# Kernel optimization log

Hardware: AMD Instinct MI355X
Metric: run time of the kernel (lower is better)

## Reference

```python
import jax, jax.numpy as jnp
import numpy as np

V, E, G = 25000, 50000, 1024
D_IN, E_IN, D, EH = 74, 12, 64, 128
STEPS, S2S, L, NT = 6, 6, 3, 1


def setup_inputs() -> dict:
    key = jax.random.key(0)
    ks = jax.random.split(key, 20)
    p = lambda k, shp: (jax.random.normal(k, shp, jnp.float32) * 0.05)
    return {
        "node_feats": jax.random.normal(ks[0], (V, D_IN), jnp.float32),
        "edge_feats": jax.random.normal(ks[1], (E, E_IN), jnp.float32),
        "src": jax.random.randint(ks[2], (E,), 0, V),
        "dst": jax.random.randint(ks[3], (E,), 0, V),
        "node2graph": jnp.sort(jax.random.randint(ks[4], (V,), 0, G)),
        "W_proj": p(ks[5], (D_IN, D)), "b_proj": jnp.zeros((D,), jnp.float32),
        "W_e1": p(ks[6], (E_IN, EH)), "b_e1": jnp.zeros((EH,), jnp.float32),
        "W_e2": p(ks[7], (EH, D * D)), "b_e2": jnp.zeros((D * D,), jnp.float32),
        "b_conv": jnp.zeros((D,), jnp.float32),
        "gru_W_ih": p(ks[8], (3 * D, D)), "gru_W_hh": p(ks[9], (3 * D, D)),
        "gru_b_ih": jnp.zeros((3 * D,), jnp.float32), "gru_b_hh": jnp.zeros((3 * D,), jnp.float32),
        "lstm_W_ih0": p(ks[10], (4 * D, 2 * D)), "lstm_W_hh0": p(ks[11], (4 * D, D)),
        "lstm_b_ih0": jnp.zeros((4 * D,), jnp.float32), "lstm_b_hh0": jnp.zeros((4 * D,), jnp.float32),
        "lstm_W_ih_r": p(ks[12], (L - 1, 4 * D, D)), "lstm_W_hh_r": p(ks[13], (L - 1, 4 * D, D)),
        "lstm_b_ih_r": jnp.zeros((L - 1, 4 * D), jnp.float32), "lstm_b_hh_r": jnp.zeros((L - 1, 4 * D), jnp.float32),
        "W1": p(ks[14], (2 * D, D)), "b1": jnp.zeros((D,), jnp.float32),
        "bn_gamma": jnp.ones((D,), jnp.float32), "bn_beta": jnp.zeros((D,), jnp.float32),
        "bn_mean": jnp.zeros((D,), jnp.float32), "bn_var": jnp.ones((D,), jnp.float32),
        "W2": p(ks[15], (D, 4 * NT)), "b2": jnp.zeros((4 * NT,), jnp.float32),
    }


def reference(node_feats, edge_feats, src, dst, node2graph,
              W_proj, b_proj, W_e1, b_e1, W_e2, b_e2, b_conv,
              gru_W_ih, gru_W_hh, gru_b_ih, gru_b_hh,
              lstm_W_ih0, lstm_W_hh0, lstm_b_ih0, lstm_b_hh0,
              lstm_W_ih_r, lstm_W_hh_r, lstm_b_ih_r, lstm_b_hh_r,
              W1, b1, bn_gamma, bn_beta, bn_mean, bn_var, W2, b2):
    # --- MPNNGNN: project + ReLU, then NNConv(sum) + ReLU + GRU, x STEPS ---
    h = jax.nn.relu(node_feats @ W_proj + b_proj)                       # (V, D)
    # edge network: per-edge (D,D) mixing matrix (edge_feats constant across steps)
    We = (jax.nn.relu(edge_feats @ W_e1 + b_e1) @ W_e2 + b_e2).reshape(E, D, D)

    def mp_step(hh, _):
        m = jnp.einsum('ed,edo->eo', hh[src], We)                       # per-edge message
        agg = jax.ops.segment_sum(m, dst, num_segments=V) + b_conv      # NNConv sum + bias
        x = jax.nn.relu(agg)
        gi = x @ gru_W_ih.T + gru_b_ih                                  # GRU (torch gate order r,z,n)
        gh = hh @ gru_W_hh.T + gru_b_hh
        ir, iz, inn = jnp.split(gi, 3, axis=-1)
        hr, hz, hn = jnp.split(gh, 3, axis=-1)
        r = jax.nn.sigmoid(ir + hr)
        z = jax.nn.sigmoid(iz + hz)
        n = jnp.tanh(inn + r * hn)
        return (1.0 - z) * n + z * hh, None

    h, _ = jax.lax.scan(mp_step, h, None, length=STEPS)

    # --- Set2Set readout ---
    q_star = jnp.zeros((G, 2 * D), h.dtype)
    hs = jnp.zeros((L, G, D), h.dtype)
    cs = jnp.zeros((L, G, D), h.dtype)
    for _ in range(S2S):
        x = q_star
        nh, nc = [], []
        for l in range(L):                                              # stacked LSTM, seq len 1
            Wih = lstm_W_ih0 if l == 0 else lstm_W_ih_r[l - 1]
            Whh = lstm_W_hh0 if l == 0 else lstm_W_hh_r[l - 1]
            bih = lstm_b_ih0 if l == 0 else lstm_b_ih_r[l - 1]
            bhh = lstm_b_hh0 if l == 0 else lstm_b_hh_r[l - 1]
            gates = x @ Wih.T + bih + hs[l] @ Whh.T + bhh               # torch order i,f,g,o
            i, f, g, o = jnp.split(gates, 4, axis=-1)
            c = jax.nn.sigmoid(f) * cs[l] + jax.nn.sigmoid(i) * jnp.tanh(g)
            hc = jax.nn.sigmoid(o) * jnp.tanh(c)
            nh.append(hc); nc.append(c)
            x = hc
        hs, cs = jnp.stack(nh), jnp.stack(nc)
        q = x                                                           # (G, D)
        e = jnp.sum(h * q[node2graph], axis=-1)                         # (V,) attention logits
        emax = jax.lax.stop_gradient(jax.ops.segment_max(e, node2graph, num_segments=G))
        emax = jnp.where(jnp.isfinite(emax), emax, 0.0)
        ez = jnp.exp(e - emax[node2graph])                              # per-graph softmax
        denom = jax.ops.segment_sum(ez, node2graph, num_segments=G)
        alpha = ez / jnp.maximum(denom[node2graph], 1e-12)
        readout = jax.ops.segment_sum(h * alpha[:, None], node2graph, num_segments=G)
        q_star = jnp.concatenate([q, readout], axis=-1)                 # (G, 2D)

    # --- evidential head: Linear + ReLU + BatchNorm(eval) + Linear ---
    h1 = jax.nn.relu(q_star @ W1 + b1)
    hbn = bn_gamma * (h1 - bn_mean) * jax.lax.rsqrt(bn_var + 1e-5) + bn_beta
    out = hbn @ W2 + b2                                                 # (G, 4*NT)
    means, logl, loga, logb = jnp.split(out, 4, axis=1)
    MINV = 1e-6
    lam = jax.nn.softplus(logl) + MINV
    alp = jax.nn.softplus(loga) + MINV + 1.0
    bet = jax.nn.softplus(logb) + MINV
    return jnp.stack([means, lam, alp, bet], axis=2).reshape(out.shape)
```

## Files before the change

kernel.cpp:

```cpp
#include <hip/hip_runtime.h>
#include <stdint.h>

#define V_N 25000
#define E_N 50000
#define G_N 1024
#define DIN 74
#define EIN 12
#define NSTEPS 6
#define NS2S 6
#define MPAD 50176

typedef unsigned int u32;
typedef unsigned short u16;
typedef __attribute__((ext_vector_type(8))) short bf16x8v;
typedef __attribute__((ext_vector_type(4))) float f32x4v;

typedef __attribute__((address_space(3))) void lds_void;
typedef __attribute__((address_space(1))) void gbl_void;

__device__ __forceinline__ void gload_lds16(const void* g, void* l) {
  __builtin_amdgcn_global_load_lds((gbl_void*)g, (lds_void*)l, 16, 0, 0);
}

__device__ __forceinline__ u16 f2bf(float f) {
  u32 u = __float_as_uint(f);
  u = (u + 0x7fffu + ((u >> 16) & 1u)) >> 16;
  return (u16)u;
}
__device__ __forceinline__ u32 pack2bf(float lo, float hi) {
  return (u32)f2bf(lo) | ((u32)f2bf(hi) << 16);
}
__device__ __forceinline__ float bflo(u32 w){ return __uint_as_float(w << 16); }
__device__ __forceinline__ float bfhi(u32 w){ return __uint_as_float(w & 0xffff0000u); }
__device__ __forceinline__ float bf2f(u16 v){ return __uint_as_float(((u32)v) << 16); }
__device__ __forceinline__ float sigf(float x){ return 1.f/(1.f + expf(-x)); }
__device__ __forceinline__ float splusf(float x){ return fmaxf(x, 0.f) + log1pf(expf(-fabsf(x))); }

__global__ void prep_kernel(const float* gWih, const float* gWhh,
                            const float* lWih0, const float* lWhh0,
                            const float* lWihr, const float* lWhhr,
                            const float* We2,
                            float* gWihT, float* gWhhT,
                            u32* TW40, u32* TU40, u32* TW4r, u32* TU4r,
                            u16* WbT) {
  int idx = blockIdx.x * 256 + threadIdx.x;
  if (idx < 12288) { int d = idx / 192, r = idx % 192; gWihT[idx] = gWih[r*64 + d]; return; }
  idx -= 12288;
  if (idx < 12288) { int d = idx / 192, r = idx % 192; gWhhT[idx] = gWhh[r*64 + d]; return; }
  idx -= 12288;
  if (idx < 16384) { int q = idx >> 2, j = idx & 3; int k8 = q >> 8, r = q & 255;
                     TW40[idx] = pack2bf(lWih0[r*128 + k8*8 + 2*j], lWih0[r*128 + k8*8 + 2*j + 1]); return; }
  idx -= 16384;
  if (idx < 8192)  { int q = idx >> 2, j = idx & 3; int k8 = q >> 8, r = q & 255;
                     TU40[idx] = pack2bf(lWhh0[r*64 + k8*8 + 2*j], lWhh0[r*64 + k8*8 + 2*j + 1]); return; }
  idx -= 8192;
  if (idx < 16384) { int l = idx >> 13, rem = idx & 8191; int q = rem >> 2, j = rem & 3;
                     int k8 = q >> 8, r = q & 255;
                     TW4r[idx] = pack2bf(lWihr[l*16384 + r*64 + k8*8 + 2*j],
                                         lWihr[l*16384 + r*64 + k8*8 + 2*j + 1]); return; }
  idx -= 16384;
  if (idx < 16384) { int l = idx >> 13, rem = idx & 8191; int q = rem >> 2, j = rem & 3;
                     int k8 = q >> 8, r = q & 255;
                     TU4r[idx] = pack2bf(lWhhr[l*16384 + r*64 + k8*8 + 2*j],
                                         lWhhr[l*16384 + r*64 + k8*8 + 2*j + 1]); return; }
  idx -= 16384;
  { int n = idx / 128, k = idx % 128; WbT[idx] = f2bf(We2[k*4096 + n]); }
}

__global__ void proj_kernel(const float* nf, const float* Wp, const float* bp, float* h) {
  int v = blockIdx.x * 4 + (threadIdx.x >> 6);
  int o = threadIdx.x & 63;
  if (v >= V_N) return;
  float acc = bp[o];
  const float* row = nf + (size_t)v * DIN;
  #pragma unroll 2
  for (int d = 0; d < DIN; ++d) acc += row[d] * Wp[d*64 + o];
  h[(size_t)v*64 + o] = fmaxf(acc, 0.f);
}

__global__ void edgenet_kernel(const float* ef, const float* W1, const float* b1, u16* zb) {
  int e = blockIdx.x * 2 + (threadIdx.x >> 7);
  int k = threadIdx.x & 127;
  float acc = 0.f;
  if (e < E_N) {
    acc = b1[k];
    const float* row = ef + (size_t)e * EIN;
    #pragma unroll
    for (int i = 0; i < EIN; ++i) acc += row[i] * W1[i*128 + k];
    acc = fmaxf(acc, 0.f);
  }
  zb[(size_t)e*128 + k] = f2bf(acc);
}

__global__ __launch_bounds__(512) void fusedmsg_kernel(const u16* zb, const u16* WbT, const float* be2,
                                                       const float* h, const int* src, const int* dst,
                                                       float* agg) {
  __shared__ __align__(16) u16 Bs[3][8192];
  __shared__ u16 hS[128][64];
  __shared__ float beS[4096];
  int t = threadIdx.x;
  int e0 = blockIdx.x * 128;
  int w = t >> 6, lane = t & 63;
  int l16 = lane & 15, lh = lane >> 4;

  #pragma unroll
  for (int it = 0; it < 8; ++it) beS[it * 512 + t] = be2[it * 512 + t];

  for (int it = 0; it < 16; ++it) {
    int idx = it * 512 + t;
    int el = idx >> 6, dd = idx & 63;
    int e = e0 + el;
    int sv = (e < E_N) ? src[e] : 0;
    hS[el][dd] = f2bf(h[(size_t)sv * 64 + dd]);
  }

  bf16x8v af[4];
  #pragma unroll
  for (int ks = 0; ks < 4; ++ks)
    af[ks] = *(const bf16x8v*)(zb + (size_t)(e0 + w*16 + l16)*128 + ks*32 + lh*8);

  #pragma unroll
  for (int pd = 0; pd < 2; ++pd) {
    const char* Bg = (const char*)(WbT + (size_t)pd * 8192);
    char* Bl = (char*)Bs[pd];
    #pragma unroll
    for (int it = 0; it < 2; ++it) {
      int f = it * 512 + t;
      int r = f >> 4, s = f & 15;
      int gc = s ^ (r & 7);
      gload_lds16(Bg + r*256 + gc*16, Bl + (size_t)(f & ~63) * 16);
    }
  }
  __syncthreads();

  float macc[4][4];
  #pragma unroll
  for (int of = 0; of < 4; ++of)
    #pragma unroll
    for (int r = 0; r < 4; ++r) macc[of][r] = 0.f;

  for (int d = 0; d < 64; ++d) {
    if (d < 62) {
      const char* Bg = (const char*)(WbT + (size_t)(d + 2) * 8192);
      char* Bl = (char*)Bs[(d + 2) % 3];
      #pragma unroll
      for (int it = 0; it < 2; ++it) {
        int f = it * 512 + t;
        int r = f >> 4, s = f & 15;
        int gc = s ^ (r & 7);
        gload_lds16(Bg + r*256 + gc*16, Bl + (size_t)(f & ~63) * 16);
      }
      asm volatile("s_waitcnt vmcnt(4)" ::: "memory");
    } else if (d == 62) {
      asm volatile("s_waitcnt vmcnt(2)" ::: "memory");
    } else {
      asm volatile("s_waitcnt vmcnt(0)" ::: "memory");
    }
    __builtin_amdgcn_s_barrier();

    float hv[4];
    #pragma unroll
    for (int r = 0; r < 4; ++r) hv[r] = bf2f(hS[w*16 + lh*4 + r][d]);

    const char* Bb = (const char*)Bs[d % 3];
    #pragma unroll
    for (int of = 0; of < 4; ++of) {
      float bias = beS[d*64 + of*16 + l16];
      f32x4v c = (f32x4v){bias, bias, bias, bias};
      #pragma unroll
      for (int ks = 0; ks < 4; ++ks) {
        int brow = of*16 + l16;
        int cb = ks*4 + lh;
        bf16x8v bf = *(const bf16x8v*)(Bb + brow*256 + ((cb ^ (brow & 7)) << 4));
        c = __builtin_amdgcn_mfma_f32_16x16x32_bf16(af[ks], bf, c, 0, 0, 0);
      }
      #pragma unroll
      for (int r = 0; r < 4; ++r) macc[of][r] += hv[r] * c[r];
    }
    asm volatile("s_waitcnt lgkmcnt(0)" ::: "memory");
    __builtin_amdgcn_s_barrier();
  }

  #pragma unroll
  for (int r = 0; r < 4; ++r) {
    int row = w*16 + lh*4 + r;
    int e = e0 + row;
    if (e < E_N) {
      int dv = dst[e];
      #pragma unroll
      for (int of = 0; of < 4; ++of)
        atomicAdd(&agg[(size_t)dv*64 + of*16 + l16], macc[of][r]);
    }
  }
}

__global__ void gru_kernel(const float* aggc, const float* bconv, const float* WihT, const float* WhhT,
                           const float* bih, const float* bhh, float* h, float* aggz) {
  int wbase = (blockIdx.x * 4 + (threadIdx.x >> 6)) * 8;
  int o = threadIdx.x & 63;
  float xv[8], hv[8];
  #pragma unroll
  for (int n = 0; n < 8; ++n) {
    int v = wbase + n;
    if (v < V_N) { xv[n] = fmaxf(aggc[(size_t)v*64 + o] + bconv[o], 0.f); hv[n] = h[(size_t)v*64 + o]; }
    else { xv[n] = 0.f; hv[n] = 0.f; }
  }
  float ar[8] = {0,0,0,0,0,0,0,0}, az[8] = {0,0,0,0,0,0,0,0}, an[8] = {0,0,0,0,0,0,0,0};
  float br[8] = {0,0,0,0,0,0,0,0}, bz[8] = {0,0,0,0,0,0,0,0}, bn2[8] = {0,0,0,0,0,0,0,0};
  #pragma unroll 4
  for (int d = 0; d < 64; ++d) {
    float wr = WihT[d*192 + o], wz = WihT[d*192 + 64 + o], wn = WihT[d*192 + 128 + o];
    float ur = WhhT[d*192 + o], uz = WhhT[d*192 + 64 + o], un = WhhT[d*192 + 128 + o];
    #pragma unroll
    for (int n = 0; n < 8; ++n) {
      float xd = __shfl(xv[n], d);
      float hd = __shfl(hv[n], d);
      ar[n] += xd*wr; az[n] += xd*wz; an[n] += xd*wn;
      br[n] += hd*ur; bz[n] += hd*uz; bn2[n] += hd*un;
    }
  }
  float b_r = bih[o] + bhh[o], b_z = bih[64+o] + bhh[64+o];
  float bin = bih[128+o], bhn = bhh[128+o];
  #pragma unroll
  for (int n = 0; n < 8; ++n) {
    int v = wbase + n;
    if (v >= V_N) continue;
    float r  = sigf(ar[n] + br[n] + b_r);
    float z  = sigf(az[n] + bz[n] + b_z);
    float nn = tanhf(an[n] + bin + r*(bn2[n] + bhn));
    h[(size_t)v*64 + o] = (1.f - z)*nn + z*hv[n];
    aggz[(size_t)v*64 + o] = 0.f;
  }
}

__global__ void gstart_kernel(const int* n2g, int* gstart) {
  int g = blockIdx.x * 256 + threadIdx.x;
  if (g > G_N) return;
  int lo = 0, hi = V_N;
  while (lo < hi) { int mid = (lo + hi) >> 1; if (n2g[mid] < g) lo = mid + 1; else hi = mid; }
  gstart[g] = lo;
}

__global__ __launch_bounds__(256) void s2s_kernel(const float* h, const int* gstart,
    const uint4* TW40, const uint4* TU40, const uint4* TW4r, const uint4* TU4r,
    const float* bih0, const float* bhh0, const float* bihr, const float* bhhr,
    float* qstar) {
  __shared__ float sq[4][128];
  __shared__ float sx[4][128];
  __shared__ float shs[4][3][64], scs[4][3][64];
  __shared__ float sg[4][256];
  int tt = threadIdx.x;
  int g0blk = blockIdx.x * 4;
  int w = tt >> 6, lane = tt & 63;
  int nstart = gstart[g0blk + w], nend = gstart[g0blk + w + 1];

  for (int i = tt; i < 512; i += 256) ((float*)sq)[i] = 0.f;
  for (int i = tt; i < 768; i += 256) { ((float*)shs)[i] = 0.f; ((float*)scs)[i] = 0.f; }
  __syncthreads();

  for (int iter = 0; iter < NS2S; ++iter) {
    for (int i = tt; i < 512; i += 256) ((float*)sx)[i] = ((float*)sq)[i];
    __syncthreads();

    for (int l = 0; l < 3; ++l) {
      const uint4* TW = (l == 0) ? TW40 : TW4r + (size_t)(l-1) * 2048;
      const uint4* TU = (l == 0) ? TU40 : TU4r + (size_t)(l-1) * 2048;
      const float* bi = (l == 0) ? bih0 : bihr + (l-1)*256;
      const float* bh = (l == 0) ? bhh0 : bhhr + (l-1)*256;
      float bsum = bi[tt] + bh[tt];
      float acc[4] = {bsum, bsum, bsum, bsum};
      if (l == 0) {
        #pragma unroll
        for (int k8 = 0; k8 < 16; ++k8) {
          uint4 u = TW[k8*256 + tt];
          #pragma unroll
          for (int gi = 0; gi < 4; ++gi) {
            const float4 xa = *(const float4*)&sx[gi][k8*8];
            const float4 xb = *(const float4*)&sx[gi][k8*8 + 4];
            acc[gi] += xa.x*bflo(u.x) + xa.y*bfhi(u.x) + xa.z*bflo(u.y) + xa.w*bfhi(u.y)
                     + xb.x*bflo(u.z) + xb.y*bfhi(u.z) + xb.z*bflo(u.w) + xb.w*bfhi(u.w);
          }
        }
      } else {
        #pragma unroll
        for (int k8 = 0; k8 < 8; ++k8) {
          uint4 u = TW[k8*256 + tt];
          #pragma unroll
          for (int gi = 0; gi < 4; ++gi) {
            const float4 xa = *(const float4*)&sx[gi][k8*8];
            const float4 xb = *(const float4*)&sx[gi][k8*8 + 4];
            acc[gi] += xa.x*bflo(u.x) + xa.y*bfhi(u.x) + xa.z*bflo(u.y) + xa.w*bfhi(u.y)
                     + xb.x*bflo(u.z) + xb.y*bfhi(u.z) + xb.z*bflo(u.w) + xb.w*bfhi(u.w);
          }
        }
      }
      #pragma unroll
      for (int k8 = 0; k8 < 8; ++k8) {
        uint4 u = TU[k8*256 + tt];
        #pragma unroll
        for (int gi = 0; gi < 4; ++gi) {
          const float4 ha = *(const float4*)&shs[gi][l][k8*8];
          const float4 hb = *(const float4*)&shs[gi][l][k8*8 + 4];
          acc[gi] += ha.x*bflo(u.x) + ha.y*bfhi(u.x) + ha.z*bflo(u.y) + ha.w*bfhi(u.y)
                   + hb.x*bflo(u.z) + hb.y*bfhi(u.z) + hb.z*bflo(u.w) + hb.w*bfhi(u.w);
        }
      }
      #pragma unroll
      for (int gi = 0; gi < 4; ++gi) sg[gi][tt] = acc[gi];
      __syncthreads();
      {
        int gq = tt >> 6, r = tt & 63;
        float gv_i = sg[gq][r], gv_f = sg[gq][64+r], gv_g = sg[gq][128+r], gv_o = sg[gq][192+r];
        float c = sigf(gv_f)*scs[gq][l][r] + sigf(gv_i)*tanhf(gv_g);
        float hc = sigf(gv_o)*tanhf(c);
        scs[gq][l][r] = c; shs[gq][l][r] = hc; sx[gq][r] = hc;
      }
      __syncthreads();
    }

    {
      float q_l = sx[w][lane];
      float lmax = -3.4e38f;
      int i = nstart;
      for (; i + 1 < nend; i += 2) {
        float h0 = h[(size_t)i*64 + lane];
        float h1 = h[(size_t)(i+1)*64 + lane];
        float v0 = h0 * q_l, v1 = h1 * q_l;
        #pragma unroll
        for (int off = 32; off; off >>= 1) { v0 += __shfl_xor(v0, off); v1 += __shfl_xor(v1, off); }
        lmax = fmaxf(lmax, fmaxf(v0, v1));
      }
      if (i < nend) {
        float h0 = h[(size_t)i*64 + lane];
        float v0 = h0 * q_l;
        #pragma unroll
        for (int off = 32; off; off >>= 1) v0 += __shfl_xor(v0, off);
        lmax = fmaxf(lmax, v0);
      }
      float lsum = 0.f, accv = 0.f;
      i = nstart;
      for (; i + 1 < nend; i += 2) {
        float h0 = h[(size_t)i*64 + lane];
        float h1 = h[(size_t)(i+1)*64 + lane];
        float v0 = h0 * q_l, v1 = h1 * q_l;
        #pragma unroll
        for (int off = 32; off; off >>= 1) { v0 += __shfl_xor(v0, off); v1 += __shfl_xor(v1, off); }
        float e0 = expf(v0 - lmax), e1 = expf(v1 - lmax);
        lsum += e0 + e1; accv += e0*h0 + e1*h1;
      }
      if (i < nend) {
        float h0 = h[(size_t)i*64 + lane];
        float v0 = h0 * q_l;
        #pragma unroll
        for (int off = 32; off; off >>= 1) v0 += __shfl_xor(v0, off);
        float e0 = expf(v0 - lmax);
        lsum += e0; accv += e0*h0;
      }
      sq[w][lane] = sx[w][lane];
      sq[w][64 + lane] = accv / fmaxf(lsum, 1e-12f);
    }
    __syncthreads();
  }

  for (int i = tt; i < 512; i += 256) qstar[(size_t)g0blk * 128 + i] = ((float*)sq)[i];
}

__global__ void head_kernel(const float* qstar, const float* W1, const float* b1,
                            const float* gma, const float* gbe, const float* gme, const float* gva,
                            const float* W2, const float* b2, float* out) {
  __shared__ float hb[4][64];
  int wslot = threadIdx.x >> 6;
  int g = blockIdx.x * 4 + wslot;
  int o = threadIdx.x & 63;
  float acc = b1[o];
  const float* q = qstar + (size_t)g * 128;
  #pragma unroll 4
  for (int k = 0; k < 128; ++k) acc += q[k] * W1[k*64 + o];
  acc = fmaxf(acc, 0.f);
  float hbn = gma[o] * (acc - gme[o]) * rsqrtf(gva[o] + 1e-5f) + gbe[o];
  hb[wslot][o] = hbn;
  __syncthreads();
  if (o < 4) {
    float v = b2[o];
    #pragma unroll 8
    for (int k = 0; k < 64; ++k) v += hb[wslot][k] * W2[k*4 + o];
    float res;
    if (o == 0) res = v;
    else { res = splusf(v) + 1e-6f; if (o == 2) res += 1.f; }
    out[(size_t)g*4 + o] = res;
  }
}

extern "C" void kernel_launch(void* const* d_in, const int* in_sizes, int n_in,
                              void* d_out, int out_size, void* d_ws, size_t ws_size,
                              hipStream_t stream) {
  const float* node_feats = (const float*)d_in[0];
  const float* edge_feats = (const float*)d_in[1];
  const int*   src        = (const int*)d_in[2];
  const int*   dst        = (const int*)d_in[3];
  const int*   n2g        = (const int*)d_in[4];
  const float* W_proj = (const float*)d_in[5];
  const float* b_proj = (const float*)d_in[6];
  const float* W_e1   = (const float*)d_in[7];
  const float* b_e1   = (const float*)d_in[8];
  const float* W_e2   = (const float*)d_in[9];
  const float* b_e2   = (const float*)d_in[10];
  const float* b_conv = (const float*)d_in[11];
  const float* gru_W_ih = (const float*)d_in[12];
  const float* gru_W_hh = (const float*)d_in[13];
  const float* gru_b_ih = (const float*)d_in[14];
  const float* gru_b_hh = (const float*)d_in[15];
  const float* lstm_W_ih0 = (const float*)d_in[16];
  const float* lstm_W_hh0 = (const float*)d_in[17];
  const float* lstm_b_ih0 = (const float*)d_in[18];
  const float* lstm_b_hh0 = (const float*)d_in[19];
  const float* lstm_W_ih_r = (const float*)d_in[20];
  const float* lstm_W_hh_r = (const float*)d_in[21];
  const float* lstm_b_ih_r = (const float*)d_in[22];
  const float* lstm_b_hh_r = (const float*)d_in[23];
  const float* W1 = (const float*)d_in[24];
  const float* b1 = (const float*)d_in[25];
  const float* bn_gamma = (const float*)d_in[26];
  const float* bn_beta  = (const float*)d_in[27];
  const float* bn_mean  = (const float*)d_in[28];
  const float* bn_var   = (const float*)d_in[29];
  const float* W2 = (const float*)d_in[30];
  const float* b2 = (const float*)d_in[31];

  char* ws = (char*)d_ws;
  size_t off = 0;
  auto alloc = [&](size_t n) { size_t c = off; off += (n + 255) & ~(size_t)255; return c; };
  u16*   zb     = (u16*)  (ws + alloc((size_t)MPAD * 128 * 2));
  float* h      = (float*)(ws + alloc((size_t)V_N * 64 * 4));
  float* agg    = (float*)(ws + alloc((size_t)V_N * 64 * 4));
  u16*   WbT    = (u16*)  (ws + alloc((size_t)4096 * 128 * 2));
  float* gWihT  = (float*)(ws + alloc(12288 * 4));
  float* gWhhT  = (float*)(ws + alloc(12288 * 4));
  u32*   TW40   = (u32*)  (ws + alloc(16384 * 4));
  u32*   TU40   = (u32*)  (ws + alloc(8192 * 4));
  u32*   TW4r   = (u32*)  (ws + alloc(16384 * 4));
  u32*   TU4r   = (u32*)  (ws + alloc(16384 * 4));
  int*   gstart = (int*)  (ws + alloc(1025 * 4));
  float* qstar  = (float*)(ws + alloc((size_t)G_N * 128 * 4));
  (void)in_sizes; (void)n_in; (void)out_size; (void)ws_size;

  prep_kernel<<<2368, 256, 0, stream>>>(gru_W_ih, gru_W_hh, lstm_W_ih0, lstm_W_hh0,
                                        lstm_W_ih_r, lstm_W_hh_r, W_e2,
                                        gWihT, gWhhT, TW40, TU40, TW4r, TU4r, WbT);
  proj_kernel<<<6250, 256, 0, stream>>>(node_feats, W_proj, b_proj, h);
  edgenet_kernel<<<MPAD / 2, 256, 0, stream>>>(edge_feats, W_e1, b_e1, zb);
  hipMemsetAsync(agg, 0, (size_t)V_N * 64 * 4, stream);

  for (int st = 0; st < NSTEPS; ++st) {
    fusedmsg_kernel<<<MPAD / 128, 512, 0, stream>>>(zb, WbT, b_e2, h, src, dst, agg);
    gru_kernel<<<782, 256, 0, stream>>>(agg, b_conv, gWihT, gWhhT, gru_b_ih, gru_b_hh, h, agg);
  }

  gstart_kernel<<<5, 256, 0, stream>>>(n2g, gstart);
  s2s_kernel<<<256, 256, 0, stream>>>(h, gstart, (const uint4*)TW40, (const uint4*)TU40,
                                      (const uint4*)TW4r, (const uint4*)TU4r,
                                      lstm_b_ih0, lstm_b_hh0, lstm_b_ih_r, lstm_b_hh_r, qstar);
  head_kernel<<<256, 256, 0, stream>>>(qstar, W1, b1, bn_gamma, bn_beta, bn_mean, bn_var,
                                       W2, b2, (float*)d_out);
}
```

Measured before the change: 1.155 ms.

## Halve fusedmsg block to 4 waves, each computing two 16-row MFMA tiles

The fused message kernel now runs 256 threads per block instead of 512. Each wave handles 32 edges (two 16-row A fragments) and reuses every B fragment read from LDS for two MFMAs, which halves LDS B traffic per MFMA. The bias table is stored as bf16 and the hS rows are padded to 66 to reduce LDS footprint and bank conflicts. Sched barriers are added around the LDS pipeline. In exchange each wave uses more registers, there are fewer waves to hide latency, and the bf16 bias adds some rounding error.

```diff
diff --git a/kernel.cpp b/kernel.cpp
--- a/kernel.cpp
+++ b/kernel.cpp
@@ -92,40 +92,42 @@
   zb[(size_t)e*128 + k] = f2bf(acc);
 }
 
-__global__ __launch_bounds__(512) void fusedmsg_kernel(const u16* zb, const u16* WbT, const float* be2,
+__global__ __launch_bounds__(256) void fusedmsg_kernel(const u16* zb, const u16* WbT, const float* be2,
                                                        const float* h, const int* src, const int* dst,
                                                        float* agg) {
   __shared__ __align__(16) u16 Bs[3][8192];
-  __shared__ u16 hS[128][64];
-  __shared__ float beS[4096];
+  __shared__ u16 hS[128][66];
+  __shared__ u16 beS[4096];
   int t = threadIdx.x;
   int e0 = blockIdx.x * 128;
   int w = t >> 6, lane = t & 63;
   int l16 = lane & 15, lh = lane >> 4;
 
   #pragma unroll
-  for (int it = 0; it < 8; ++it) beS[it * 512 + t] = be2[it * 512 + t];
-
-  for (int it = 0; it < 16; ++it) {
-    int idx = it * 512 + t;
+  for (int it = 0; it < 16; ++it) beS[it * 256 + t] = f2bf(be2[it * 256 + t]);
+
+  for (int it = 0; it < 32; ++it) {
+    int idx = it * 256 + t;
     int el = idx >> 6, dd = idx & 63;
     int e = e0 + el;
     int sv = (e < E_N) ? src[e] : 0;
     hS[el][dd] = f2bf(h[(size_t)sv * 64 + dd]);
   }
 
-  bf16x8v af[4];
-  #pragma unroll
-  for (int ks = 0; ks < 4; ++ks)
-    af[ks] = *(const bf16x8v*)(zb + (size_t)(e0 + w*16 + l16)*128 + ks*32 + lh*8);
+  bf16x8v af[2][4];
+  #pragma unroll
+  for (int rf = 0; rf < 2; ++rf)
+    #pragma unroll
+    for (int ks = 0; ks < 4; ++ks)
+      af[rf][ks] = *(const bf16x8v*)(zb + (size_t)(e0 + w*32 + rf*16 + l16)*128 + ks*32 + lh*8);
 
   #pragma unroll
   for (int pd = 0; pd < 2; ++pd) {
     const char* Bg = (const char*)(WbT + (size_t)pd * 8192);
     char* Bl = (char*)Bs[pd];
     #pragma unroll
-    for (int it = 0; it < 2; ++it) {
-      int f = it * 512 + t;
+    for (int it = 0; it < 4; ++it) {
+      int f = it * 256 + t;
       int r = f >> 4, s = f & 15;
       int gc = s ^ (r & 7);
       gload_lds16(Bg + r*256 + gc*16, Bl + (size_t)(f & ~63) * 16);
@@ -133,65 +135,79 @@
   }
   __syncthreads();
 
-  float macc[4][4];
-  #pragma unroll
-  for (int of = 0; of < 4; ++of)
-    #pragma unroll
-    for (int r = 0; r < 4; ++r) macc[of][r] = 0.f;
+  float macc[2][4][4];
+  #pragma unroll
+  for (int rf = 0; rf < 2; ++rf)
+    #pragma unroll
+    for (int of = 0; of < 4; ++of)
+      #pragma unroll
+      for (int r = 0; r < 4; ++r) macc[rf][of][r] = 0.f;
 
   for (int d = 0; d < 64; ++d) {
     if (d < 62) {
       const char* Bg = (const char*)(WbT + (size_t)(d + 2) * 8192);
       char* Bl = (char*)Bs[(d + 2) % 3];
       #pragma unroll
-      for (int it = 0; it < 2; ++it) {
-        int f = it * 512 + t;
+      for (int it = 0; it < 4; ++it) {
+        int f = it * 256 + t;
         int r = f >> 4, s = f & 15;
         int gc = s ^ (r & 7);
         gload_lds16(Bg + r*256 + gc*16, Bl + (size_t)(f & ~63) * 16);
       }
+      asm volatile("s_waitcnt vmcnt(8)" ::: "memory");
+    } else if (d == 62) {
       asm volatile("s_waitcnt vmcnt(4)" ::: "memory");
-    } else if (d == 62) {
-      asm volatile("s_waitcnt vmcnt(2)" ::: "memory");
     } else {
       asm volatile("s_waitcnt vmcnt(0)" ::: "memory");
     }
     __builtin_amdgcn_s_barrier();
-
-    float hv[4];
-    #pragma unroll
-    for (int r = 0; r < 4; ++r) hv[r] = bf2f(hS[w*16 + lh*4 + r][d]);
+    __builtin_amdgcn_sched_barrier(0);
+
+    float hv[2][4];
+    #pragma unroll
+    for (int rf = 0; rf < 2; ++rf)
+      #pragma unroll
+      for (int r = 0; r < 4; ++r)
+        hv[rf][r] = bf2f(hS[w*32 + rf*16 + lh*4 + r][d]);
 
     const char* Bb = (const char*)Bs[d % 3];
     #pragma unroll
     for (int of = 0; of < 4; ++of) {
-      float bias = beS[d*64 + of*16 + l16];
-      f32x4v c = (f32x4v){bias, bias, bias, bias};
+      float bias = bf2f(beS[d*64 + of*16 + l16]);
+      f32x4v c0 = (f32x4v){bias, bias, bias, bias};
+      f32x4v c1 = c0;
       #pragma unroll
       for (int ks = 0; ks < 4; ++ks) {
         int brow = of*16 + l16;
         int cb = ks*4 + lh;
         bf16x8v bf = *(const bf16x8v*)(Bb + brow*256 + ((cb ^ (brow & 7)) << 4));
-        c = __builtin_amdgcn_mfma_f32_16x16x32_bf16(af[ks], bf, c, 0, 0, 0);
-      }
-      #pragma unroll
-      for (int r = 0; r < 4; ++r) macc[of][r] += hv[r] * c[r];
+        c0 = __builtin_amdgcn_mfma_f32_16x16x32_bf16(af[0][ks], bf, c0, 0, 0, 0);
+        c1 = __builtin_amdgcn_mfma_f32_16x16x32_bf16(af[1][ks], bf, c1, 0, 0, 0);
+      }
+      #pragma unroll
+      for (int r = 0; r < 4; ++r) {
+        macc[0][of][r] += hv[0][r] * c0[r];
+        macc[1][of][r] += hv[1][r] * c1[r];
+      }
     }
     asm volatile("s_waitcnt lgkmcnt(0)" ::: "memory");
+    __builtin_amdgcn_sched_barrier(0);
     __builtin_amdgcn_s_barrier();
   }
 
   #pragma unroll
-  for (int r = 0; r < 4; ++r) {
-    int row = w*16 + lh*4 + r;
-    int e = e0 + row;
-    if (e < E_N) {
-      int dv = dst[e];
-      #pragma unroll
-      for (int of = 0; of < 4; ++of)
-        atomicAdd(&agg[(size_t)dv*64 + of*16 + l16], macc[of][r]);
-    }
-  }
+  for (int rf = 0; rf < 2; ++rf)
+    #pragma unroll
+    for (int r = 0; r < 4; ++r) {
+      int row = w*32 + rf*16 + lh*4 + r;
+      int e = e0 + row;
+      if (e < E_N) {
+        int dv = dst[e];
+        #pragma unroll
+        for (int of = 0; of < 4; ++of)
+          atomicAdd(&agg[(size_t)dv*64 + of*16 + l16], macc[rf][of][r]);
+      }
+    }
 }
 
 __global__ void gru_kernel(const float* aggc, const float* bconv, const float* WihT, const float* WhhT,
@@ -452,7 +468,7 @@
   hipMemsetAsync(agg, 0, (size_t)V_N * 64 * 4, stream);
 
   for (int st = 0; st < NSTEPS; ++st) {
-    fusedmsg_kernel<<<MPAD / 128, 512, 0, stream>>>(zb, WbT, b_e2, h, src, dst, agg);
+    fusedmsg_kernel<<<MPAD / 128, 256, 0, stream>>>(zb, WbT, b_e2, h, src, dst, agg);
     gru_kernel<<<782, 256, 0, stream>>>(agg, b_conv, gWihT, gWhhT, gru_b_ih, gru_b_hh, h, agg);
   }
 
```

Result: faster. 1.127 ms (-2.4%).
